# Performance work log

Measured on AMD Instinct MI355X. Metric: run time of the kernel, lower is better.

Reference implementation:

```python
import jax, jax.numpy as jnp
import numpy as np

NEG_SLOPE = 0.2   # PyG GATConv default negative_slope
LN_EPS = 1e-5
SOFTMAX_EPS = 1e-16  # PyG softmax denominator eps


def setup_inputs() -> dict:
    key = jax.random.key(0)
    ks = jax.random.split(key, 6)
    N, IN, OUT, H, E = 100000, 128, 64, 2, 1600000
    X = jax.random.normal(ks[0], (N, IN), dtype=jnp.float32)
    edge_index = jax.random.randint(ks[1], (2, E), 0, N, dtype=jnp.int64)
    W = jax.random.normal(ks[2], (H * OUT, IN), dtype=jnp.float32) * 0.05
    att_src = jax.random.normal(ks[3], (H, OUT), dtype=jnp.float32) * 0.05
    att_dst = jax.random.normal(ks[4], (H, OUT), dtype=jnp.float32) * 0.05
    bias = jnp.zeros((OUT,), dtype=jnp.float32)
    ln_gamma = jnp.ones((OUT,), dtype=jnp.float32)
    ln_beta = jnp.zeros((OUT,), dtype=jnp.float32)
    return {"X": X, "edge_index": edge_index, "W": W, "att_src": att_src,
            "att_dst": att_dst, "bias": bias, "ln_gamma": ln_gamma, "ln_beta": ln_beta}


def reference(X, edge_index, W, att_src, att_dst, bias, ln_gamma, ln_beta):
    N = X.shape[0]
    H, F = att_src.shape
    # PyG GATConv default: add self-loops
    loops = jnp.arange(N, dtype=edge_index.dtype)
    src = jnp.concatenate([edge_index[0], loops])  # [Et]
    dst = jnp.concatenate([edge_index[1], loops])  # [Et]
    # linear projection: x' = X @ W^T  -> [N, H, F]
    x = (X @ W.T).reshape(N, H, F)
    # per-node attention logits  [N, H]
    a_src = jnp.einsum('nhf,hf->nh', x, att_src)
    a_dst = jnp.einsum('nhf,hf->nh', x, att_dst)
    # per-edge logits, leaky relu  [Et, H]
    e = jax.nn.leaky_relu(a_src[src] + a_dst[dst], NEG_SLOPE)
    # segment softmax over incoming edges of each dst node
    m = jax.ops.segment_max(e, dst, num_segments=N)          # [N, H]
    ex = jnp.exp(e - m[dst])
    denom = jax.ops.segment_sum(ex, dst, num_segments=N)     # [N, H]
    alpha = ex / (denom[dst] + SOFTMAX_EPS)                  # [Et, H]
    # weighted scatter-add of source features
    msg = x[src] * alpha[:, :, None]                         # [Et, H, F]
    out = jax.ops.segment_sum(msg, dst, num_segments=N)      # [N, H, F]
    # concat=False -> mean over heads, then bias
    out = out.mean(axis=1) + bias                            # [N, F]
    # LayerNorm over features
    mu = out.mean(axis=-1, keepdims=True)
    var = ((out - mu) ** 2).mean(axis=-1, keepdims=True)
    h = (out - mu) * jax.lax.rsqrt(var + LN_EPS) * ln_gamma + ln_beta
    return h
```

## Files before the change

### kernel.cpp

```cpp
#include <hip/hip_runtime.h>
#include <hip/hip_bf16.h>

#define NEG_SLOPE 0.2f
#define LN_EPS 1e-5f
#define SM_EPS 1e-16f

typedef __attribute__((ext_vector_type(8))) short bf16x8;
typedef __attribute__((ext_vector_type(4))) float f32x4;

__device__ inline unsigned short f2bf(float f) {
    unsigned u = __float_as_uint(f);
    return (unsigned short)((u + 0x7FFFu + ((u >> 16) & 1u)) >> 16);
}
__device__ inline float bf_lo(unsigned int v) { return __uint_as_float(v << 16); }
__device__ inline float bf_hi(unsigned int v) { return __uint_as_float(v & 0xffff0000u); }

#define NBIN 1024
#define BCAP 2560
#define SCHUNK 2048

__global__ __launch_bounds__(256) void k_gemm(const float* __restrict__ X,
                                              const float* __restrict__ W,
                                              const float* __restrict__ att_src,
                                              const float* __restrict__ att_dst,
                                              unsigned int* __restrict__ xp,
                                              float2* __restrict__ aS,
                                              float2* __restrict__ aD,
                                              int* __restrict__ binCursor, int N) {
    __shared__ unsigned short Ws[128 * 136];
    __shared__ unsigned short Xs[64 * 136];
    const int t = threadIdx.x;
    const int b0 = blockIdx.x * 64;
    const int lane = t & 63;
    const int w = t >> 6;
    const int c15 = lane & 15;
    const int quad = lane >> 4;

    if (blockIdx.x == 0) {
        for (int i = t; i < NBIN; i += 256) binCursor[i] = i * BCAP;
    }

#pragma unroll
    for (int i = 0; i < 16; ++i) {
        int f = i * 256 + t;
        int nr = f >> 5;
        int q = f & 31;
        float4 v = reinterpret_cast<const float4*>(W)[nr * 32 + q];
        ushort4 b;
        b.x = f2bf(v.x); b.y = f2bf(v.y); b.z = f2bf(v.z); b.w = f2bf(v.w);
        *reinterpret_cast<ushort4*>(&Ws[nr * 136 + q * 4]) = b;
    }
#pragma unroll
    for (int i = 0; i < 8; ++i) {
        int f = i * 256 + t;
        int m = f >> 5;
        int q = f & 31;
        int gr = b0 + m;
        if (gr >= N) gr = N - 1;
        float4 v = reinterpret_cast<const float4*>(X)[(size_t)gr * 32 + q];
        ushort4 b;
        b.x = f2bf(v.x); b.y = f2bf(v.y); b.z = f2bf(v.z); b.w = f2bf(v.w);
        *reinterpret_cast<ushort4*>(&Xs[m * 136 + q * 4]) = b;
    }
    __syncthreads();

    f32x4 acc[8];
#pragma unroll
    for (int ct = 0; ct < 8; ++ct) acc[ct] = (f32x4){0.f, 0.f, 0.f, 0.f};

#pragma unroll
    for (int kc = 0; kc < 4; ++kc) {
        bf16x8 af = *reinterpret_cast<const bf16x8*>(
            &Xs[(w * 16 + c15) * 136 + kc * 32 + quad * 8]);
#pragma unroll
        for (int ct = 0; ct < 8; ++ct) {
            bf16x8 bfr = *reinterpret_cast<const bf16x8*>(
                &Ws[(ct * 16 + c15) * 136 + kc * 32 + quad * 8]);
            acc[ct] = __builtin_amdgcn_mfma_f32_16x16x32_bf16(af, bfr, acc[ct], 0, 0, 0);
        }
    }

    float attS[8], attD[8];
#pragma unroll
    for (int ct = 0; ct < 8; ++ct) {
        attS[ct] = att_src[ct * 16 + c15];
        attD[ct] = att_dst[ct * 16 + c15];
    }

#pragma unroll
    for (int r = 0; r < 4; ++r) {
        int row = b0 + w * 16 + quad * 4 + r;
        float s0 = 0.f, s1 = 0.f, d0 = 0.f, d1 = 0.f;
#pragma unroll
        for (int ct = 0; ct < 4; ++ct) {
            s0 += acc[ct][r] * attS[ct];
            d0 += acc[ct][r] * attD[ct];
            s1 += acc[ct + 4][r] * attS[ct + 4];
            d1 += acc[ct + 4][r] * attD[ct + 4];
        }
#pragma unroll
        for (int o = 1; o < 16; o <<= 1) {
            s0 += __shfl_xor(s0, o);
            s1 += __shfl_xor(s1, o);
            d0 += __shfl_xor(d0, o);
            d1 += __shfl_xor(d1, o);
        }
        if (row < N) {
#pragma unroll
            for (int ct = 0; ct < 4; ++ct) {
                unsigned int p = (unsigned int)f2bf(acc[ct][r]) |
                                 ((unsigned int)f2bf(acc[ct + 4][r]) << 16);
                xp[(size_t)row * 64 + ct * 16 + c15] = p;
            }
            if (c15 == 0) {
                aS[row] = make_float2(s0, s1);
                aD[row] = make_float2(d0, d1);
            }
        }
    }
}

__global__ __launch_bounds__(256) void k_scatter(const int* __restrict__ ei,
                                                 const float2* __restrict__ aS,
                                                 const float2* __restrict__ aD,
                                                 int* __restrict__ binCursor,
                                                 uint2* __restrict__ tmp, int E) {
    __shared__ int off[NBIN];
    const int t = threadIdx.x;
    const int base = blockIdx.x * SCHUNK;

    int se[8], de[8];
    unsigned int ue[8];
#pragma unroll
    for (int k = 0; k < 8; ++k) {
        int i = base + k * 256 + t;
        if (i < E) {
            int s = ei[i];
            int d = ei[E + i];
            se[k] = s; de[k] = d;
            float2 a = aS[s];
            float2 ad2 = aD[d];
            float f0 = a.x + ad2.x; f0 = fmaxf(f0, NEG_SLOPE * f0);
            float f1 = a.y + ad2.y; f1 = fmaxf(f1, NEG_SLOPE * f1);
            ue[k] = (unsigned int)f2bf(__expf(f0)) |
                    ((unsigned int)f2bf(__expf(f1)) << 16);
        } else {
            de[k] = -1;
        }
    }

    for (int i = t; i < NBIN; i += 256) off[i] = 0;
    __syncthreads();
#pragma unroll
    for (int k = 0; k < 8; ++k)
        if (de[k] >= 0) atomicAdd(&off[de[k] >> 7], 1);
    __syncthreads();
    for (int i = t; i < NBIN; i += 256) {
        int h = off[i];
        off[i] = h ? atomicAdd(&binCursor[i], h) : 0;
    }
    __syncthreads();
#pragma unroll
    for (int k = 0; k < 8; ++k) {
        if (de[k] >= 0) {
            int p = atomicAdd(&off[de[k] >> 7], 1);
            tmp[p] = make_uint2(((unsigned)(de[k] & 127) << 24) | (unsigned)se[k],
                                ue[k]);
        }
    }
}

__global__ __launch_bounds__(256) void k_bucket(const uint2* __restrict__ tmp,
                                                const int* __restrict__ binCursor,
                                                const float2* __restrict__ aS,
                                                const float2* __restrict__ aD,
                                                uint2* __restrict__ csr,
                                                unsigned int* __restrict__ rowPtr,
                                                float4* __restrict__ metaN, int N) {
    __shared__ uint2 ebuf[BCAP];
    __shared__ int cnt[128];
    __shared__ int cur[128];
    __shared__ float den0[128], den1[128];
    __shared__ int lds2[2];
    const int t = threadIdx.x;
    const int b = blockIdx.x;
    const int start = b * BCAP;
    int m = binCursor[b] - start;
    if (m > BCAP) m = BCAP;

    if (t < 128) { cnt[t] = 0; den0[t] = 0.f; den1[t] = 0.f; }
    __syncthreads();

    for (int k = t; k < m; k += 256) {
        uint2 e = tmp[start + k];
        ebuf[k] = e;
        int li = e.x >> 24;
        atomicAdd(&cnt[li], 1);
        atomicAdd(&den0[li], bf_lo(e.y));
        atomicAdd(&den1[li], bf_hi(e.y));
    }
    __syncthreads();

    int v = 0, incl = 0;
    const int lane = t & 63, w = t >> 6;
    if (t < 128) {
        v = cnt[t];
        incl = v;
#pragma unroll
        for (int o = 1; o < 64; o <<= 1) {
            int u = __shfl_up(incl, o);
            if (lane >= o) incl += u;
        }
        if (lane == 63) lds2[w] = incl;
    }
    __syncthreads();
    if (t == 0) { int a = lds2[0]; lds2[0] = 0; lds2[1] = a; }
    __syncthreads();
    if (t < 128) {
        int excl = lds2[w] + incl - v;
        cur[t] = excl;
        int d = b * 128 + t;
        if (d < N) {
            float2 a = aS[d];
            float2 ad2 = aD[d];
            float f0 = a.x + ad2.x; f0 = fmaxf(f0, NEG_SLOPE * f0);
            float f1 = a.y + ad2.y; f1 = fmaxf(f1, NEG_SLOPE * f1);
            float ws0 = __expf(f0), ws1 = __expf(f1);
            float D0 = den0[t] + ws0, D1 = den1[t] + ws1;
            metaN[d] = make_float4(ws0, ws1,
                                   0.5f / (D0 + SM_EPS), 0.5f / (D1 + SM_EPS));
            rowPtr[d] = (unsigned)(start + excl) | ((unsigned)v << 22);
        }
    }
    __syncthreads();

    for (int k = t; k < m; k += 256) {
        uint2 e = ebuf[k];
        int li = e.x >> 24;
        int p = atomicAdd(&cur[li], 1);
        csr[start + p] = make_uint2(e.x & 0x00FFFFFFu, e.y);
    }
}

__global__ __launch_bounds__(256) void k_agg(const unsigned int* __restrict__ xp,
                                             const float4* __restrict__ metaN,
                                             const unsigned int* __restrict__ rowPtr,
                                             const uint2* __restrict__ csr,
                                             const float* __restrict__ bias,
                                             const float* __restrict__ gamma,
                                             const float* __restrict__ beta,
                                             float* __restrict__ out, int N) {
    const int w = threadIdx.x >> 6, lane = threadIdx.x & 63;
    const int n = blockIdx.x * 4 + w;
    if (n >= N) return;

    float4 meta = metaN[n];
    unsigned int vself = xp[(size_t)n * 64 + lane];
    float S0 = meta.x * bf_lo(vself);
    float S1 = meta.y * bf_hi(vself);

    unsigned int pr = rowPtr[n];
    const int jb = (int)(pr & 0x3FFFFFu);
    const int je = jb + (int)(pr >> 22);
    int j = jb;
    for (; j + 7 < je; j += 8) {
        int ju = __builtin_amdgcn_readfirstlane(j);
        uint2 c[8];
#pragma unroll
        for (int q = 0; q < 8; ++q) c[q] = csr[ju + q];
        unsigned int v[8];
#pragma unroll
        for (int q = 0; q < 8; ++q) v[q] = xp[(size_t)c[q].x * 64 + lane];
#pragma unroll
        for (int q = 0; q < 8; ++q) {
            S0 += bf_lo(c[q].y) * bf_lo(v[q]);
            S1 += bf_hi(c[q].y) * bf_hi(v[q]);
        }
    }
    for (; j + 3 < je; j += 4) {
        int ju = __builtin_amdgcn_readfirstlane(j);
        uint2 c[4];
#pragma unroll
        for (int q = 0; q < 4; ++q) c[q] = csr[ju + q];
        unsigned int v[4];
#pragma unroll
        for (int q = 0; q < 4; ++q) v[q] = xp[(size_t)c[q].x * 64 + lane];
#pragma unroll
        for (int q = 0; q < 4; ++q) {
            S0 += bf_lo(c[q].y) * bf_lo(v[q]);
            S1 += bf_hi(c[q].y) * bf_hi(v[q]);
        }
    }
    for (; j < je; ++j) {
        uint2 c = csr[__builtin_amdgcn_readfirstlane(j)];
        unsigned int vv = xp[(size_t)c.x * 64 + lane];
        S0 += bf_lo(c.y) * bf_lo(vv);
        S1 += bf_hi(c.y) * bf_hi(vv);
    }

    float o = meta.z * S0 + meta.w * S1 + bias[lane];

    float mu = o;
#pragma unroll
    for (int d = 32; d > 0; d >>= 1) mu += __shfl_xor(mu, d);
    mu *= (1.0f / 64.0f);
    float dv = o - mu;
    float var = dv * dv;
#pragma unroll
    for (int d = 32; d > 0; d >>= 1) var += __shfl_xor(var, d);
    var *= (1.0f / 64.0f);
    out[(size_t)n * 64 + lane] = dv * rsqrtf(var + LN_EPS) * gamma[lane] + beta[lane];
}

extern "C" void kernel_launch(void* const* d_in, const int* in_sizes, int n_in,
                              void* d_out, int out_size, void* d_ws, size_t ws_size,
                              hipStream_t stream) {
    const float* X        = (const float*)d_in[0];
    const int*   ei       = (const int*)d_in[1];
    const float* W        = (const float*)d_in[2];
    const float* att_src  = (const float*)d_in[3];
    const float* att_dst  = (const float*)d_in[4];
    const float* bias     = (const float*)d_in[5];
    const float* ln_gamma = (const float*)d_in[6];
    const float* ln_beta  = (const float*)d_in[7];
    float* out = (float*)d_out;

    const int N = in_sizes[0] / 128;
    const int E = in_sizes[1] / 2;
    const int NBUCK = (N + 127) / 128;

    char* ws = (char*)d_ws;
    size_t off = 0;
    auto alloc = [&](size_t bytes) {
        size_t o = off;
        off += (bytes + 255) & ~(size_t)255;
        return o;
    };
    unsigned int* xp     = (unsigned int*)(ws + alloc((size_t)N * 64 * 4));
    float2* aS           = (float2*)(ws + alloc((size_t)N * 8));
    float2* aD           = (float2*)(ws + alloc((size_t)N * 8));
    float4* metaN        = (float4*)(ws + alloc((size_t)N * 16));
    unsigned int* rowPtr = (unsigned int*)(ws + alloc((size_t)N * 4));
    uint2* csr           = (uint2*)(ws + alloc((size_t)NBIN * BCAP * 8));
    uint2* tmp           = (uint2*)(ws + alloc((size_t)NBIN * BCAP * 8));
    int* binCursor       = (int*)(ws + alloc(NBIN * 4));

    k_gemm<<<(N + 63) / 64, 256, 0, stream>>>(X, W, att_src, att_dst, xp, aS, aD,
                                              binCursor, N);
    k_scatter<<<(E + SCHUNK - 1) / SCHUNK, 256, 0, stream>>>(ei, aS, aD,
                                                             binCursor, tmp, E);
    k_bucket<<<NBUCK, 256, 0, stream>>>(tmp, binCursor, aS, aD, csr, rowPtr,
                                        metaN, N);
    k_agg<<<(N + 3) / 4, 256, 0, stream>>>(xp, metaN, rowPtr, csr,
                                           bias, ln_gamma, ln_beta, out, N);
}
```

Measured before the change: 252.6 us.

## Use 256-node bins, pad bin cursors, double scatter chunk, drop LDS edge buffer

Bins now cover 256 destination nodes each (512 bins instead of 1024), and each scatter block handles 4096 edges, so fewer global atomics hit the bin cursors. The cursors are spaced 16 ints apart so concurrent atomics fall on different cache lines. The bucket kernel no longer stages edges in LDS; it reads tmp from global memory twice, which frees LDS for occupancy. In exchange it adds global reread traffic and heavier per-bin contention, and the bucket grid shrinks to about 391 blocks.

Measured after the change: 245.2 us. -2.9%, faster.

```diff
diff --git a/kernel.cpp b/kernel.cpp
--- a/kernel.cpp
+++ b/kernel.cpp
@@ -15,9 +15,10 @@
 __device__ inline float bf_lo(unsigned int v) { return __uint_as_float(v << 16); }
 __device__ inline float bf_hi(unsigned int v) { return __uint_as_float(v & 0xffff0000u); }
 
-#define NBIN 1024
-#define BCAP 2560
-#define SCHUNK 2048
+#define NBIN 512
+#define BCAP 4864
+#define SCHUNK 4096
+#define CURPAD 16
 
 __global__ __launch_bounds__(256) void k_gemm(const float* __restrict__ X,
                                               const float* __restrict__ W,
@@ -37,7 +38,7 @@
     const int quad = lane >> 4;
 
     if (blockIdx.x == 0) {
-        for (int i = t; i < NBIN; i += 256) binCursor[i] = i * BCAP;
+        for (int i = t; i < NBIN; i += 256) binCursor[i * CURPAD] = i * BCAP;
     }
 
 #pragma unroll
@@ -129,10 +130,10 @@
     const int t = threadIdx.x;
     const int base = blockIdx.x * SCHUNK;
 
-    int se[8], de[8];
-    unsigned int ue[8];
-#pragma unroll
-    for (int k = 0; k < 8; ++k) {
+    int se[16], de[16];
+    unsigned int ue[16];
+#pragma unroll
+    for (int k = 0; k < 16; ++k) {
         int i = base + k * 256 + t;
         if (i < E) {
             int s = ei[i];
@@ -152,19 +153,19 @@
     for (int i = t; i < NBIN; i += 256) off[i] = 0;
     __syncthreads();
 #pragma unroll
-    for (int k = 0; k < 8; ++k)
-        if (de[k] >= 0) atomicAdd(&off[de[k] >> 7], 1);
+    for (int k = 0; k < 16; ++k)
+        if (de[k] >= 0) atomicAdd(&off[de[k] >> 8], 1);
     __syncthreads();
     for (int i = t; i < NBIN; i += 256) {
         int h = off[i];
-        off[i] = h ? atomicAdd(&binCursor[i], h) : 0;
-    }
-    __syncthreads();
-#pragma unroll
-    for (int k = 0; k < 8; ++k) {
+        off[i] = h ? atomicAdd(&binCursor[i * CURPAD], h) : 0;
+    }
+    __syncthreads();
+#pragma unroll
+    for (int k = 0; k < 16; ++k) {
         if (de[k] >= 0) {
-            int p = atomicAdd(&off[de[k] >> 7], 1);
-            tmp[p] = make_uint2(((unsigned)(de[k] & 127) << 24) | (unsigned)se[k],
+            int p = atomicAdd(&off[de[k] >> 8], 1);
+            tmp[p] = make_uint2(((unsigned)(de[k] & 255) << 24) | (unsigned)se[k],
                                 ue[k]);
         }
     }
@@ -177,23 +178,21 @@
                                                 uint2* __restrict__ csr,
                                                 unsigned int* __restrict__ rowPtr,
                                                 float4* __restrict__ metaN, int N) {
-    __shared__ uint2 ebuf[BCAP];
-    __shared__ int cnt[128];
-    __shared__ int cur[128];
-    __shared__ float den0[128], den1[128];
-    __shared__ int lds2[2];
+    __shared__ int cnt[256];
+    __shared__ int cur[256];
+    __shared__ float den0[256], den1[256];
+    __shared__ int lds[4];
     const int t = threadIdx.x;
     const int b = blockIdx.x;
     const int start = b * BCAP;
-    int m = binCursor[b] - start;
+    int m = binCursor[b * CURPAD] - start;
     if (m > BCAP) m = BCAP;
 
-    if (t < 128) { cnt[t] = 0; den0[t] = 0.f; den1[t] = 0.f; }
+    cnt[t] = 0; den0[t] = 0.f; den1[t] = 0.f;
     __syncthreads();
 
     for (int k = t; k < m; k += 256) {
         uint2 e = tmp[start + k];
-        ebuf[k] = e;
         int li = e.x >> 24;
         atomicAdd(&cnt[li], 1);
         atomicAdd(&den0[li], bf_lo(e.y));
@@ -201,41 +200,40 @@
     }
     __syncthreads();
 
-    int v = 0, incl = 0;
+    int v = cnt[t];
     const int lane = t & 63, w = t >> 6;
-    if (t < 128) {
-        v = cnt[t];
-        incl = v;
-#pragma unroll
-        for (int o = 1; o < 64; o <<= 1) {
-            int u = __shfl_up(incl, o);
-            if (lane >= o) incl += u;
-        }
-        if (lane == 63) lds2[w] = incl;
-    }
-    __syncthreads();
-    if (t == 0) { int a = lds2[0]; lds2[0] = 0; lds2[1] = a; }
-    __syncthreads();
-    if (t < 128) {
-        int excl = lds2[w] + incl - v;
-        cur[t] = excl;
-        int d = b * 128 + t;
-        if (d < N) {
-            float2 a = aS[d];
-            float2 ad2 = aD[d];
-            float f0 = a.x + ad2.x; f0 = fmaxf(f0, NEG_SLOPE * f0);
-            float f1 = a.y + ad2.y; f1 = fmaxf(f1, NEG_SLOPE * f1);
-            float ws0 = __expf(f0), ws1 = __expf(f1);
-            float D0 = den0[t] + ws0, D1 = den1[t] + ws1;
-            metaN[d] = make_float4(ws0, ws1,
-                                   0.5f / (D0 + SM_EPS), 0.5f / (D1 + SM_EPS));
-            rowPtr[d] = (unsigned)(start + excl) | ((unsigned)v << 22);
-        }
+    int incl = v;
+#pragma unroll
+    for (int o = 1; o < 64; o <<= 1) {
+        int u = __shfl_up(incl, o);
+        if (lane >= o) incl += u;
+    }
+    if (lane == 63) lds[w] = incl;
+    __syncthreads();
+    if (t == 0) {
+        int run = 0;
+        for (int i = 0; i < 4; ++i) { int tv = lds[i]; lds[i] = run; run += tv; }
+    }
+    __syncthreads();
+    int excl = lds[w] + incl - v;
+    cur[t] = excl;
+
+    int d = b * 256 + t;
+    if (d < N) {
+        float2 a = aS[d];
+        float2 ad2 = aD[d];
+        float f0 = a.x + ad2.x; f0 = fmaxf(f0, NEG_SLOPE * f0);
+        float f1 = a.y + ad2.y; f1 = fmaxf(f1, NEG_SLOPE * f1);
+        float ws0 = __expf(f0), ws1 = __expf(f1);
+        float D0 = den0[t] + ws0, D1 = den1[t] + ws1;
+        metaN[d] = make_float4(ws0, ws1,
+                               0.5f / (D0 + SM_EPS), 0.5f / (D1 + SM_EPS));
+        rowPtr[d] = (unsigned)(start + excl) | ((unsigned)v << 22);
     }
     __syncthreads();
 
     for (int k = t; k < m; k += 256) {
-        uint2 e = ebuf[k];
+        uint2 e = tmp[start + k];
         int li = e.x >> 24;
         int p = atomicAdd(&cur[li], 1);
         csr[start + p] = make_uint2(e.x & 0x00FFFFFFu, e.y);
@@ -327,7 +325,7 @@
 
     const int N = in_sizes[0] / 128;
     const int E = in_sizes[1] / 2;
-    const int NBUCK = (N + 127) / 128;
+    const int NBUCK = (N + 255) / 256;
 
     char* ws = (char*)d_ws;
     size_t off = 0;
@@ -343,7 +341,7 @@
     unsigned int* rowPtr = (unsigned int*)(ws + alloc((size_t)N * 4));
     uint2* csr           = (uint2*)(ws + alloc((size_t)NBIN * BCAP * 8));
     uint2* tmp           = (uint2*)(ws + alloc((size_t)NBIN * BCAP * 8));
-    int* binCursor       = (int*)(ws + alloc(NBIN * 4));
+    int* binCursor       = (int*)(ws + alloc(NBIN * CURPAD * 4));
 
     k_gemm<<<(N + 63) / 64, 256, 0, stream>>>(X, W, att_src, att_dst, xp, aS, aD,
                                               binCursor, N);
```
